# Optimization experiments

Measured on AMD Instinct MI355X. Metric: run time of the kernel, lower is better.

The kernel has to match this reference:

```python
import jax, jax.numpy as jnp
import numpy as np

N_DOMAIN = 10
DOM_EMB = 4
IN_DIM = 1024
HIDDEN = [1024, 512, 256]
N_EXPERTS = 8
LORA_R = 16


def _glorot(key, shape):
    fan_in, fan_out = shape[-2], shape[-1]
    lim = np.sqrt(6.0 / (fan_in + fan_out))
    return jax.random.uniform(key, shape, jnp.float32, -lim, lim)


def setup_inputs() -> dict:
    key = jax.random.key(0)
    ks = jax.random.split(key, 32)
    inp = {
        "dnn_input": jax.random.normal(ks[0], (16384, IN_DIM), jnp.float32),
        "domain_input": jax.random.randint(ks[1], (16384,), 0, N_DOMAIN, jnp.int64),
        "emb_table": jax.random.normal(ks[2], (N_DOMAIN, DOM_EMB), jnp.float32),
        "gate_W": _glorot(ks[3], (DOM_EMB, N_EXPERTS)),
        "gate_b": jnp.zeros((N_EXPERTS,), jnp.float32),
    }
    prev = IN_DIM
    k = 4
    for li, h in enumerate(HIDDEN):
        inp[f"W{li}"] = _glorot(ks[k], (prev, h)); k += 1
        inp[f"b{li}"] = jnp.zeros((h,), jnp.float32)
        # original inits B and lora_bias to zeros; use small randoms so outputs/grads are non-trivial
        inp[f"A{li}"] = _glorot(ks[k], (N_EXPERTS, prev, LORA_R)); k += 1
        inp[f"B{li}"] = 0.01 * jax.random.normal(ks[k], (N_EXPERTS, LORA_R, h), jnp.float32); k += 1
        inp[f"lb{li}"] = 0.01 * jax.random.normal(ks[k], (N_EXPERTS, h), jnp.float32); k += 1
        prev = h
    return inp


def _moe_layer(x, gate, W, b, A, B, lb):
    # base GEMM (dropout is identity: rate 0 / inference)
    base = x @ W + b                                   # [B, h]
    t = jnp.einsum('bp,epr->ber', x, A)                # [B, E, r]
    eo = jnp.einsum('ber,erh->beh', t, B) + lb[None]   # [B, E, h]
    moe = jnp.einsum('be,beh->bh', gate, eo)           # [B, h]
    return jax.nn.relu(base + moe)


def reference(dnn_input, domain_input, emb_table, gate_W, gate_b,
              W0, b0, A0, B0, lb0,
              W1, b1, A1, B1, lb1,
              W2, b2, A2, B2, lb2):
    dom = emb_table[domain_input]                      # [B, 4]
    gate = jax.nn.softmax(dom @ gate_W + gate_b, axis=-1)  # [B, E]
    x = dnn_input
    x = _moe_layer(x, gate, W0, b0, A0, B0, lb0)
    x = _moe_layer(x, gate, W1, b1, A1, B1, lb1)
    x = _moe_layer(x, gate, W2, b2, A2, B2, lb2)
    return x
```

## Files before the change

kernel.cpp:

```cpp
#include <hip/hip_runtime.h>
#include <hip/hip_bf16.h>
#include <stdint.h>

#define KAUG 192
#define M_ROWS 16384

typedef __attribute__((ext_vector_type(8))) __bf16 bf16x8;
typedef __attribute__((ext_vector_type(4))) float f32x4;

__device__ __forceinline__ unsigned short f2b(float f) {
  unsigned int u = __builtin_bit_cast(unsigned int, f);
  u = (u + 0x7fffu + ((u >> 16) & 1u)) >> 16;
  return (unsigned short)u;
}

__device__ __forceinline__ void lds_load16(const unsigned short* g, unsigned short* l) {
  __builtin_amdgcn_global_load_lds(
      (const __attribute__((address_space(1))) void*)g,
      (__attribute__((address_space(3))) void*)l, 16, 0, 0);
}

template<int N> __device__ __forceinline__ void vmcnt_wait() {
  if constexpr (N == 0)      asm volatile("s_waitcnt vmcnt(0)" ::: "memory");
  else if constexpr (N == 3) asm volatile("s_waitcnt vmcnt(3)" ::: "memory");
  else if constexpr (N == 4) asm volatile("s_waitcnt vmcnt(4)" ::: "memory");
  else if constexpr (N == 6) asm volatile("s_waitcnt vmcnt(6)" ::: "memory");
  else                       asm volatile("s_waitcnt vmcnt(8)" ::: "memory");
}


__global__ void gate_aug_kernel(const int* __restrict__ dom, const float* __restrict__ emb,
                                const float* __restrict__ gW, const float* __restrict__ gb,
                                float* __restrict__ gate, unsigned short* __restrict__ tg) {
  int i = blockIdx.x * blockDim.x + threadIdx.x;
  int d = dom[i];
  float e0 = emb[d*4+0], e1 = emb[d*4+1], e2 = emb[d*4+2], e3 = emb[d*4+3];
  float l[8]; float mx = -1e30f;
#pragma unroll
  for (int j = 0; j < 8; j++) {
    l[j] = e0*gW[j] + e1*gW[8+j] + e2*gW[16+j] + e3*gW[24+j] + gb[j];
    mx = fmaxf(mx, l[j]);
  }
  float s = 0.f;
#pragma unroll
  for (int j = 0; j < 8; j++) { l[j] = __expf(l[j] - mx); s += l[j]; }
  float inv = 1.0f / s;
  unsigned int g[4];
#pragma unroll
  for (int j = 0; j < 8; j++) {
    float v = l[j] * inv;
    gate[i*8+j] = v;
    unsigned int b = f2b(v);
    if (j & 1) g[j >> 1] |= b << 16; else g[j >> 1] = b;
  }
  uint4* dst = (uint4*)&tg[(long)i * KAUG + 128];
  dst[0] = make_uint4(g[0], g[1], g[2], g[3]);
  uint4 z4 = make_uint4(0, 0, 0, 0);
#pragma unroll
  for (int q = 1; q < 8; q++) dst[q] = z4;
}

__global__ void f32_to_bf16_vec(const float* __restrict__ in, unsigned int* __restrict__ out, long n8) {
  long i = (long)blockIdx.x * blockDim.x + threadIdx.x;
  if (i >= n8) return;
  float4 a = ((const float4*)in)[i * 2];
  float4 b = ((const float4*)in)[i * 2 + 1];
  uint4 o;
  o.x = f2b(a.x) | ((unsigned)f2b(a.y) << 16);
  o.y = f2b(a.z) | ((unsigned)f2b(a.w) << 16);
  o.z = f2b(b.x) | ((unsigned)f2b(b.y) << 16);
  o.w = f2b(b.z) | ((unsigned)f2b(b.w) << 16);
  ((uint4*)out)[i] = o;
}

__global__ void build_wt_all(const float* __restrict__ w0, const float* __restrict__ w1,
                             const float* __restrict__ w2,
                             unsigned short* __restrict__ t0, unsigned short* __restrict__ t1,
                             unsigned short* __restrict__ t2) {
  int z = blockIdx.z;
  const float* W = z == 0 ? w0 : (z == 1 ? w1 : w2);
  unsigned short* Wt = z == 0 ? t0 : (z == 1 ? t1 : t2);
  int K = (z == 2) ? 512 : 1024;
  int N = (z == 0) ? 1024 : (z == 1 ? 512 : 256);
  int n0 = blockIdx.x * 32, k0 = blockIdx.y * 32;
  if (n0 >= N || k0 >= K) return;
  __shared__ float tl[32][33];
  int tx = threadIdx.x & 31, ty = threadIdx.x >> 5;
#pragma unroll
  for (int i = 0; i < 32; i += 8)
    tl[ty + i][tx] = W[(long)(k0 + ty + i) * N + n0 + tx];
  __syncthreads();
#pragma unroll
  for (int i = 0; i < 32; i += 8)
    Wt[(long)(n0 + ty + i) * K + k0 + tx] = f2b(tl[tx][ty + i]);
}

__global__ void build_aft_all(const float* __restrict__ a0, const float* __restrict__ a1,
                              const float* __restrict__ a2,
                              unsigned short* __restrict__ t0, unsigned short* __restrict__ t1,
                              unsigned short* __restrict__ t2) {
  int z = blockIdx.z;
  const float* A = z == 0 ? a0 : (z == 1 ? a1 : a2);
  unsigned short* Aft = z == 0 ? t0 : (z == 1 ? t1 : t2);
  int P = (z == 2) ? 512 : 1024;
  long p0 = (long)blockIdx.x * 64;
  if (p0 >= P) return;
  int e = blockIdx.y;
  __shared__ float tl[64][17];
  int t = threadIdx.x;
#pragma unroll
  for (int pass = 0; pass < 4; pass++) {
    int idx = t + pass * 256;
    int pl = idx >> 4, r = idx & 15;
    tl[pl][r] = A[((long)e * P + p0 + pl) * 16 + r];
  }
  __syncthreads();
#pragma unroll
  for (int pass = 0; pass < 4; pass++) {
    int idx = t + pass * 256;
    int r = idx >> 6, pl = idx & 63;
    Aft[(long)(e * 16 + r) * P + p0 + pl] = f2b(tl[pl][r]);
  }
}

__global__ void build_bft_all(const float* __restrict__ b0, const float* __restrict__ b1,
                              const float* __restrict__ b2,
                              const float* __restrict__ l0, const float* __restrict__ l1,
                              const float* __restrict__ l2,
                              unsigned short* __restrict__ t0, unsigned short* __restrict__ t1,
                              unsigned short* __restrict__ t2) {
  int z = blockIdx.z;
  const float* Bm = z == 0 ? b0 : (z == 1 ? b1 : b2);
  const float* lb = z == 0 ? l0 : (z == 1 ? l1 : l2);
  unsigned short* Bft = z == 0 ? t0 : (z == 1 ? t1 : t2);
  int H = (z == 0) ? 1024 : (z == 1 ? 512 : 256);
  int n0 = blockIdx.x * 32, kk0 = blockIdx.y * 32;
  if (n0 >= H) return;
  __shared__ float tl[32][33];
  int tx = threadIdx.x & 31, ty = threadIdx.x >> 5;
#pragma unroll
  for (int i = 0; i < 32; i += 8) {
    int kk = kk0 + ty + i;
    float v;
    if (kk < 128)       v = Bm[(long)kk * H + n0 + tx];
    else if (kk < 136)  v = lb[(long)(kk - 128) * H + n0 + tx];
    else                v = 0.f;
    tl[ty + i][tx] = v;
  }
  __syncthreads();
#pragma unroll
  for (int i = 0; i < 32; i += 8)
    Bft[(long)(n0 + ty + i) * KAUG + kk0 + tx] = f2b(tl[tx][ty + i]);
}

template<int MODE, int BM>
__global__ __launch_bounds__(512)
void gemm_mn(const unsigned short* __restrict__ A1, int lda1, int K1,
             const unsigned short* __restrict__ A2, int lda2, int K2,
             const unsigned short* __restrict__ Bt1, int ldb1,
             const unsigned short* __restrict__ Bt2, int ldb2,
             const float* __restrict__ bias,
             const float* __restrict__ gate,
             void* __restrict__ outp, int ldout) {
  constexpr int MFRAG = BM / 32;
  constexpr int ATOT = BM * 64;
  constexpr int BTOT = 128 * 64;
  constexpr int LA = BM / 64;
  constexpr int L = LA + 2;
  __shared__ __attribute__((aligned(16))) unsigned short lds[3 * ATOT + 3 * BTOT];

  const int t = threadIdx.x;
  const int lane = t & 63, wave = t >> 6;
  const int wr = wave >> 2, wc = wave & 3;
  const int rl = lane & 15, kg = lane >> 4;
  const int row0 = blockIdx.x * BM, col0 = blockIdx.y * 128;

  const int sr = t >> 3;
  const int sk = ((t & 7) ^ (sr & 7)) * 8;

  f32x4 acc[MFRAG][2];
#pragma unroll
  for (int m = 0; m < MFRAG; m++)
#pragma unroll
    for (int n = 0; n < 2; n++) acc[m][n] = (f32x4){0.f, 0.f, 0.f, 0.f};

  auto stageA = [&](int buf, int kt) {
    const unsigned short* src; long ld; int kl;
    if (kt < K1) { src = A1; ld = lda1; kl = kt; }
    else         { src = A2; ld = lda2; kl = kt - K1; }
    unsigned short* d = &lds[buf * ATOT + t * 8];
    const unsigned short* s = src + (long)(row0 + sr) * ld + kl + sk;
#pragma unroll
    for (int i = 0; i < LA; i++)
      lds_load16(s + (long)(i * 64) * ld, d + i * 4096);
  };
  auto stageB = [&](int buf, int kt) {
    const unsigned short* src; long ld; int kl;
    if (kt < K1) { src = Bt1; ld = ldb1; kl = kt; }
    else         { src = Bt2; ld = ldb2; kl = kt - K1; }
    unsigned short* d = &lds[3 * ATOT + buf * BTOT + t * 8];
    const unsigned short* s = src + (long)(col0 + sr) * ld + kl + sk;
    lds_load16(s, d);
    lds_load16(s + 64 * ld, d + 4096);
  };
  auto ldA = [&](int buf, int mg, int ks) {
    int lr = wr * (BM / 2) + mg * 16 + rl;
    int sc = (ks * 4 + kg) ^ (lr & 7);
    return *(const bf16x8*)&lds[buf * ATOT + lr * 64 + sc * 8];
  };
  auto ldB = [&](int buf, int n, int ks) {
    int cr = wc * 32 + n * 16 + rl;
    int sc = (ks * 4 + kg) ^ (cr & 7);
    return *(const bf16x8*)&lds[3 * ATOT + buf * BTOT + cr * 64 + sc * 8];
  };

  const int Ktot = K1 + K2;
  const int NT = Ktot / 64;

  stageA(0, 0); stageB(0, 0);
  stageA(1, 64); stageB(1, 64);
  vmcnt_wait<L>();
  __builtin_amdgcn_s_barrier();

  int bcur = 0;
  bf16x8 Bfv[2][2];
  for (int tt = 0; tt < NT; ++tt) {
    int bpf = bcur + 2; if (bpf > 2) bpf -= 3;
    const bool pf = (tt + 2 < NT);
    bf16x8 Af[(MFRAG + 1) / 2][2];
#pragma unroll
    for (int m = 0; m < MFRAG / 2; m++) { Af[m][0] = ldA(bcur, m, 0); Af[m][1] = ldA(bcur, m, 1); }
#pragma unroll
    for (int n = 0; n < 2; n++) { Bfv[n][0] = ldB(bcur, n, 0); Bfv[n][1] = ldB(bcur, n, 1); }
    if (pf) stageA(bpf, (tt + 2) * 64);
    __builtin_amdgcn_s_barrier();
    asm volatile("s_waitcnt lgkmcnt(0)" ::: "memory");
    __builtin_amdgcn_sched_barrier(0);
    __builtin_amdgcn_s_setprio(1);
#pragma unroll
    for (int m = 0; m < MFRAG / 2; m++)
#pragma unroll
      for (int n = 0; n < 2; n++) {
        acc[m][n] = __builtin_amdgcn_mfma_f32_16x16x32_bf16(Af[m][0], Bfv[n][0], acc[m][n], 0, 0, 0);
        acc[m][n] = __builtin_amdgcn_mfma_f32_16x16x32_bf16(Af[m][1], Bfv[n][1], acc[m][n], 0, 0, 0);
      }
    __builtin_amdgcn_s_setprio(0);
    __builtin_amdgcn_s_barrier();
#pragma unroll
    for (int m = 0; m < MFRAG / 2; m++) { Af[m][0] = ldA(bcur, MFRAG / 2 + m, 0); Af[m][1] = ldA(bcur, MFRAG / 2 + m, 1); }
    if (pf) stageB(bpf, (tt + 2) * 64);
    if (tt + 1 < NT) vmcnt_wait<L>();
    else             vmcnt_wait<0>();
    __builtin_amdgcn_s_barrier();
    asm volatile("s_waitcnt lgkmcnt(0)" ::: "memory");
    __builtin_amdgcn_sched_barrier(0);
    __builtin_amdgcn_s_setprio(1);
#pragma unroll
    for (int m = 0; m < MFRAG / 2; m++)
#pragma unroll
      for (int n = 0; n < 2; n++) {
        acc[MFRAG / 2 + m][n] = __builtin_amdgcn_mfma_f32_16x16x32_bf16(Af[m][0], Bfv[n][0], acc[MFRAG / 2 + m][n], 0, 0, 0);
        acc[MFRAG / 2 + m][n] = __builtin_amdgcn_mfma_f32_16x16x32_bf16(Af[m][1], Bfv[n][1], acc[MFRAG / 2 + m][n], 0, 0, 0);
      }
    __builtin_amdgcn_s_setprio(0);
    __builtin_amdgcn_s_barrier();
    bcur = bcur == 2 ? 0 : bcur + 1;
  }

#pragma unroll
  for (int m = 0; m < MFRAG; m++)
#pragma unroll
    for (int n = 0; n < 2; n++)
#pragma unroll
      for (int j = 0; j < 4; j++) {
        int row = row0 + wr * (BM / 2) + m * 16 + kg * 4 + j;
        int col = col0 + wc * 32 + n * 16 + rl;
        float v = acc[m][n][j];
        if (MODE == 0) {
          v *= gate[row * 8 + (col >> 4)];
          ((unsigned short*)outp)[(long)row * ldout + col] = f2b(v);
        } else {
          v += bias[col];
          v = fmaxf(v, 0.f);
          if (MODE == 1) ((unsigned short*)outp)[(long)row * ldout + col] = f2b(v);
          else           ((float*)outp)[(long)row * ldout + col] = v;
        }
      }
}

template<int MODE, int BM>
__global__ __launch_bounds__(256, 4)
void gemm2b(const unsigned short* __restrict__ A1, int lda1, int K1,
            const unsigned short* __restrict__ A2, int lda2, int K2,
            const unsigned short* __restrict__ Bt1, int ldb1,
            const unsigned short* __restrict__ Bt2, int ldb2,
            const float* __restrict__ bias,
            const float* __restrict__ gate,
            void* __restrict__ outp, int ldout) {
  constexpr int ATOT = BM * 64;
  constexpr int BTOT = 128 * 64;
  constexpr int MF = BM / 64;
  constexpr int LA = BM / 32;
  __shared__ __attribute__((aligned(16))) unsigned short lds[2 * ATOT + 2 * BTOT];

  const int t = threadIdx.x;
  const int lane = t & 63, wave = t >> 6;
  const int wr = wave >> 1, wc = wave & 1;
  const int rl = lane & 15, kg = lane >> 4;
  const int row0 = blockIdx.x * BM, col0 = blockIdx.y * 128;

  const int sr = t >> 3;
  const int sk = ((t & 7) ^ (sr & 7)) * 8;

  f32x4 acc[2 * MF][4];
#pragma unroll
  for (int m = 0; m < 2 * MF; m++)
#pragma unroll
    for (int n = 0; n < 4; n++) acc[m][n] = (f32x4){0.f, 0.f, 0.f, 0.f};

  auto stageA = [&](int buf, int kt) {
    const unsigned short* src; long ld; int kl;
    if (kt < K1) { src = A1; ld = lda1; kl = kt; }
    else         { src = A2; ld = lda2; kl = kt - K1; }
    unsigned short* d = &lds[buf * ATOT + t * 8];
    const unsigned short* s = src + (long)(row0 + sr) * ld + kl + sk;
#pragma unroll
    for (int i = 0; i < LA; i++)
      lds_load16(s + (long)(i * 32) * ld, d + i * 2048);
  };
  auto stageB = [&](int buf, int kt) {
    const unsigned short* src; long ld; int kl;
    if (kt < K1) { src = Bt1; ld = ldb1; kl = kt; }
    else         { src = Bt2; ld = ldb2; kl = kt - K1; }
    unsigned short* d = &lds[2 * ATOT + buf * BTOT + t * 8];
    const unsigned short* s = src + (long)(col0 + sr) * ld + kl + sk;
#pragma unroll
    for (int i = 0; i < 4; i++)
      lds_load16(s + (long)(i * 32) * ld, d + i * 2048);
  };
  auto ldA = [&](int buf, int mf, int ks) {
    int lr = wr * (BM / 2) + mf * 16 + rl;
    int sc = (ks * 4 + kg) ^ (lr & 7);
    return *(const bf16x8*)&lds[buf * ATOT + lr * 64 + sc * 8];
  };
  auto ldB = [&](int buf, int nf, int ks) {
    int cr = wc * 64 + nf * 16 + rl;
    int sc = (ks * 4 + kg) ^ (cr & 7);
    return *(const bf16x8*)&lds[2 * ATOT + buf * BTOT + cr * 64 + sc * 8];
  };

  const int NT = (K1 + K2) / 64;

  stageA(0, 0); stageB(0, 0);
  asm volatile("s_waitcnt vmcnt(0)" ::: "memory");
  __builtin_amdgcn_s_barrier();

  int cur = 0;
  for (int tt = 0; tt < NT; ++tt) {
    const bool pf = (tt + 1 < NT);
    const int kt1 = (tt + 1) * 64;
    if (pf) { stageA(cur ^ 1, kt1); stageB(cur ^ 1, kt1); }
    bf16x8 Am_[MF][2], Bf[4][2];
#pragma unroll
    for (int mf = 0; mf < MF; mf++) { Am_[mf][0] = ldA(cur, mf, 0); Am_[mf][1] = ldA(cur, mf, 1); }
#pragma unroll
    for (int nf = 0; nf < 4; nf++) { Bf[nf][0] = ldB(cur, nf, 0); Bf[nf][1] = ldB(cur, nf, 1); }
    asm volatile("s_waitcnt lgkmcnt(0)" ::: "memory");
    __builtin_amdgcn_sched_barrier(0);
    __builtin_amdgcn_s_setprio(1);
#pragma unroll
    for (int mf = 0; mf < MF; mf++)
#pragma unroll
      for (int nf = 0; nf < 4; nf++) {
        acc[mf][nf] = __builtin_amdgcn_mfma_f32_16x16x32_bf16(Am_[mf][0], Bf[nf][0], acc[mf][nf], 0, 0, 0);
        acc[mf][nf] = __builtin_amdgcn_mfma_f32_16x16x32_bf16(Am_[mf][1], Bf[nf][1], acc[mf][nf], 0, 0, 0);
      }
    __builtin_amdgcn_s_setprio(0);
#pragma unroll
    for (int mf = 0; mf < MF; mf++) { Am_[mf][0] = ldA(cur, MF + mf, 0); Am_[mf][1] = ldA(cur, MF + mf, 1); }
    asm volatile("s_waitcnt lgkmcnt(0)" ::: "memory");
    __builtin_amdgcn_sched_barrier(0);
    __builtin_amdgcn_s_setprio(1);
#pragma unroll
    for (int mf = 0; mf < MF; mf++)
#pragma unroll
      for (int nf = 0; nf < 4; nf++) {
        acc[MF + mf][nf] = __builtin_amdgcn_mfma_f32_16x16x32_bf16(Am_[mf][0], Bf[nf][0], acc[MF + mf][nf], 0, 0, 0);
        acc[MF + mf][nf] = __builtin_amdgcn_mfma_f32_16x16x32_bf16(Am_[mf][1], Bf[nf][1], acc[MF + mf][nf], 0, 0, 0);
      }
    __builtin_amdgcn_s_setprio(0);
    if (pf) asm volatile("s_waitcnt vmcnt(0)" ::: "memory");
    __builtin_amdgcn_s_barrier();
    cur ^= 1;
  }

#pragma unroll
  for (int m = 0; m < 2 * MF; m++)
#pragma unroll
    for (int n = 0; n < 4; n++)
#pragma unroll
      for (int j = 0; j < 4; j++) {
        int row = row0 + wr * (BM / 2) + m * 16 + kg * 4 + j;
        int col = col0 + wc * 64 + n * 16 + rl;
        float v = acc[m][n][j];
        if (MODE == 0) {
          v *= gate[row * 8 + (col >> 4)];
          ((unsigned short*)outp)[(long)row * ldout + col] = f2b(v);
        } else {
          v += bias[col];
          v = fmaxf(v, 0.f);
          if (MODE == 1) ((unsigned short*)outp)[(long)row * ldout + col] = f2b(v);
          else           ((float*)outp)[(long)row * ldout + col] = v;
        }
      }
}


extern "C" void kernel_launch(void* const* d_in, const int* in_sizes, int n_in,
                              void* d_out, int out_size, void* d_ws, size_t ws_size,
                              hipStream_t stream) {
  (void)in_sizes; (void)n_in; (void)out_size; (void)ws_size;
  const float* dnn = (const float*)d_in[0];
  const int*   dom = (const int*)d_in[1];
  const float* emb = (const float*)d_in[2];
  const float* gW  = (const float*)d_in[3];
  const float* gb  = (const float*)d_in[4];
  const float* Wm[3]  = {(const float*)d_in[5],  (const float*)d_in[10], (const float*)d_in[15]};
  const float* bm[3]  = {(const float*)d_in[6],  (const float*)d_in[11], (const float*)d_in[16]};
  const float* Am[3]  = {(const float*)d_in[7],  (const float*)d_in[12], (const float*)d_in[17]};
  const float* Bm[3]  = {(const float*)d_in[8],  (const float*)d_in[13], (const float*)d_in[18]};
  const float* lbm[3] = {(const float*)d_in[9],  (const float*)d_in[14], (const float*)d_in[19]};

  const int M = M_ROWS;
  const int dIn[3]  = {1024, 1024, 512};
  const int dOutN[3] = {1024, 512, 256};

  char* p = (char*)d_ws;
  auto carve = [&](size_t bytes) { char* r = p; p += (bytes + 255) & ~(size_t)255; return r; };
  float* gate = (float*)carve((size_t)M * 8 * sizeof(float));
  unsigned short* xb0 = (unsigned short*)carve((size_t)M * 1024 * 2);
  unsigned short* xb1 = (unsigned short*)carve((size_t)M * 1024 * 2);
  unsigned short* tg  = (unsigned short*)carve((size_t)M * KAUG * 2);
  unsigned short *Wt[3], *Aft[3], *Bft[3];
  for (int l = 0; l < 3; l++) {
    Wt[l]  = (unsigned short*)carve((size_t)dOutN[l] * dIn[l] * 2);
    Aft[l] = (unsigned short*)carve((size_t)128 * dIn[l] * 2);
    Bft[l] = (unsigned short*)carve((size_t)dOutN[l] * KAUG * 2);
  }

  gate_aug_kernel<<<M / 256, 256, 0, stream>>>(dom, emb, gW, gb, gate, tg);
  {
    long n8 = (long)M * 1024 / 8;
    f32_to_bf16_vec<<<(int)((n8 + 255) / 256), 256, 0, stream>>>(dnn, (unsigned int*)xb0, n8);
  }
  build_wt_all<<<dim3(32, 32, 3), 256, 0, stream>>>(Wm[0], Wm[1], Wm[2], Wt[0], Wt[1], Wt[2]);
  build_aft_all<<<dim3(16, 8, 3), 256, 0, stream>>>(Am[0], Am[1], Am[2], Aft[0], Aft[1], Aft[2]);
  build_bft_all<<<dim3(32, KAUG / 32, 3), 256, 0, stream>>>(Bm[0], Bm[1], Bm[2],
                                                            lbm[0], lbm[1], lbm[2],
                                                            Bft[0], Bft[1], Bft[2]);

  const unsigned short* xin = xb0;
  for (int l = 0; l < 3; l++) {
    int K1 = dIn[l], N = dOutN[l];
    gemm_mn<0, 64><<<dim3(M / 64, 1), 512, 0, stream>>>(
        xin, K1, K1, nullptr, 0, 0, Aft[l], K1, nullptr, 0, nullptr, gate, (void*)tg, KAUG);
    if (l == 0)
      gemm2b<1, 128><<<dim3(M / 128, N / 128), 256, 0, stream>>>(
          xin, K1, K1, tg, KAUG, KAUG, Wt[l], K1, Bft[l], KAUG, bm[l], nullptr, (void*)xb1, N);
    else if (l == 1)
      gemm2b<1, 128><<<dim3(M / 128, N / 128), 256, 0, stream>>>(
          xin, K1, K1, tg, KAUG, KAUG, Wt[l], K1, Bft[l], KAUG, bm[l], nullptr, (void*)xb0, N);
    else
      gemm2b<2, 64><<<dim3(M / 64, N / 128), 256, 0, stream>>>(
          xin, K1, K1, tg, KAUG, KAUG, Wt[l], K1, Bft[l], KAUG, bm[l], nullptr, d_out, N);
    xin = (l == 0) ? xb1 : xb0;
  }
}
```

Before: 139.7 us.

## Fuse fp32-to-bf16 input conversion into layer-0 GEMM A-tile staging

Removes the standalone fp32-to-bf16 conversion kernel for the input and instead has both layer-0 GEMMs (LoRA-A projection and base+LoRA-B GEMM) load fp32 rows, convert them in registers, and store bf16 into LDS. This is meant to eliminate the intermediate bf16 buffer write/read and one launch. In exchange, the A-tile staging becomes synchronous register-path loads with full __syncthreads instead of async global-to-LDS loads, occupancy is lowered, and the fp32 input is read at double width by multiple column blocks.

```diff
diff --git a/kernel.cpp b/kernel.cpp
--- a/kernel.cpp
+++ b/kernel.cpp
@@ -58,19 +58,6 @@
   uint4 z4 = make_uint4(0, 0, 0, 0);
 #pragma unroll
   for (int q = 1; q < 8; q++) dst[q] = z4;
-}
-
-__global__ void f32_to_bf16_vec(const float* __restrict__ in, unsigned int* __restrict__ out, long n8) {
-  long i = (long)blockIdx.x * blockDim.x + threadIdx.x;
-  if (i >= n8) return;
-  float4 a = ((const float4*)in)[i * 2];
-  float4 b = ((const float4*)in)[i * 2 + 1];
-  uint4 o;
-  o.x = f2b(a.x) | ((unsigned)f2b(a.y) << 16);
-  o.y = f2b(a.z) | ((unsigned)f2b(a.w) << 16);
-  o.z = f2b(b.x) | ((unsigned)f2b(b.y) << 16);
-  o.w = f2b(b.z) | ((unsigned)f2b(b.w) << 16);
-  ((uint4*)out)[i] = o;
 }
 
 __global__ void build_wt_all(const float* __restrict__ w0, const float* __restrict__ w1,
@@ -288,15 +275,16 @@
       }
 }
 
-template<int MODE, int BM>
-__global__ __launch_bounds__(256, 4)
+template<int MODE, int BM, bool F32A>
+__global__ __launch_bounds__(256, F32A ? 2 : 4)
 void gemm2b(const unsigned short* __restrict__ A1, int lda1, int K1,
             const unsigned short* __restrict__ A2, int lda2, int K2,
             const unsigned short* __restrict__ Bt1, int ldb1,
             const unsigned short* __restrict__ Bt2, int ldb2,
             const float* __restrict__ bias,
             const float* __restrict__ gate,
-            void* __restrict__ outp, int ldout) {
+            void* __restrict__ outp, int ldout,
+            const float* __restrict__ Af32) {
   constexpr int ATOT = BM * 64;
   constexpr int BTOT = 128 * 64;
   constexpr int MF = BM / 64;
@@ -319,10 +307,28 @@
     for (int n = 0; n < 4; n++) acc[m][n] = (f32x4){0.f, 0.f, 0.f, 0.f};
 
   auto stageA = [&](int buf, int kt) {
+    unsigned short* d = &lds[buf * ATOT + t * 8];
+    if constexpr (F32A) {
+      if (kt < K1) {
+        const float* s = Af32 + (long)(row0 + sr) * lda1 + kt + sk;
+#pragma unroll
+        for (int i = 0; i < LA; i++) {
+          const float* sp = s + (long)(i * 32) * lda1;
+          float4 a = *(const float4*)sp;
+          float4 b = *(const float4*)(sp + 4);
+          uint4 o;
+          o.x = f2b(a.x) | ((unsigned)f2b(a.y) << 16);
+          o.y = f2b(a.z) | ((unsigned)f2b(a.w) << 16);
+          o.z = f2b(b.x) | ((unsigned)f2b(b.y) << 16);
+          o.w = f2b(b.z) | ((unsigned)f2b(b.w) << 16);
+          *(uint4*)(d + i * 2048) = o;
+        }
+        return;
+      }
+    }
     const unsigned short* src; long ld; int kl;
     if (kt < K1) { src = A1; ld = lda1; kl = kt; }
     else         { src = A2; ld = lda2; kl = kt - K1; }
-    unsigned short* d = &lds[buf * ATOT + t * 8];
     const unsigned short* s = src + (long)(row0 + sr) * ld + kl + sk;
 #pragma unroll
     for (int i = 0; i < LA; i++)
@@ -352,8 +358,7 @@
   const int NT = (K1 + K2) / 64;
 
   stageA(0, 0); stageB(0, 0);
-  asm volatile("s_waitcnt vmcnt(0)" ::: "memory");
-  __builtin_amdgcn_s_barrier();
+  __syncthreads();
 
   int cur = 0;
   for (int tt = 0; tt < NT; ++tt) {
@@ -389,8 +394,12 @@
         acc[MF + mf][nf] = __builtin_amdgcn_mfma_f32_16x16x32_bf16(Am_[mf][1], Bf[nf][1], acc[MF + mf][nf], 0, 0, 0);
       }
     __builtin_amdgcn_s_setprio(0);
-    if (pf) asm volatile("s_waitcnt vmcnt(0)" ::: "memory");
-    __builtin_amdgcn_s_barrier();
+    if constexpr (F32A) {
+      __syncthreads();
+    } else {
+      if (pf) asm volatile("s_waitcnt vmcnt(0)" ::: "memory");
+      __builtin_amdgcn_s_barrier();
+    }
     cur ^= 1;
   }
 
@@ -449,30 +458,26 @@
   }
 
   gate_aug_kernel<<<M / 256, 256, 0, stream>>>(dom, emb, gW, gb, gate, tg);
-  {
-    long n8 = (long)M * 1024 / 8;
-    f32_to_bf16_vec<<<(int)((n8 + 255) / 256), 256, 0, stream>>>(dnn, (unsigned int*)xb0, n8);
-  }
   build_wt_all<<<dim3(32, 32, 3), 256, 0, stream>>>(Wm[0], Wm[1], Wm[2], Wt[0], Wt[1], Wt[2]);
   build_aft_all<<<dim3(16, 8, 3), 256, 0, stream>>>(Am[0], Am[1], Am[2], Aft[0], Aft[1], Aft[2]);
   build_bft_all<<<dim3(32, KAUG / 32, 3), 256, 0, stream>>>(Bm[0], Bm[1], Bm[2],
                                                             lbm[0], lbm[1], lbm[2],
                                                             Bft[0], Bft[1], Bft[2]);
 
-  const unsigned short* xin = xb0;
-  for (int l = 0; l < 3; l++) {
-    int K1 = dIn[l], N = dOutN[l];
-    gemm_mn<0, 64><<<dim3(M / 64, 1), 512, 0, stream>>>(
-        xin, K1, K1, nullptr, 0, 0, Aft[l], K1, nullptr, 0, nullptr, gate, (void*)tg, KAUG);
-    if (l == 0)
-      gemm2b<1, 128><<<dim3(M / 128, N / 128), 256, 0, stream>>>(
-          xin, K1, K1, tg, KAUG, KAUG, Wt[l], K1, Bft[l], KAUG, bm[l], nullptr, (void*)xb1, N);
-    else if (l == 1)
-      gemm2b<1, 128><<<dim3(M / 128, N / 128), 256, 0, stream>>>(
-          xin, K1, K1, tg, KAUG, KAUG, Wt[l], K1, Bft[l], KAUG, bm[l], nullptr, (void*)xb0, N);
-    else
-      gemm2b<2, 64><<<dim3(M / 64, N / 128), 256, 0, stream>>>(
-          xin, K1, K1, tg, KAUG, KAUG, Wt[l], K1, Bft[l], KAUG, bm[l], nullptr, d_out, N);
-    xin = (l == 0) ? xb1 : xb0;
-  }
-}
+  gemm2b<0, 64, true><<<dim3(M / 64, 1), 256, 0, stream>>>(
+      nullptr, 1024, 1024, nullptr, 0, 0, Aft[0], 1024, nullptr, 0,
+      nullptr, gate, (void*)tg, KAUG, dnn);
+  gemm2b<1, 128, true><<<dim3(M / 128, 1024 / 128), 256, 0, stream>>>(
+      nullptr, 1024, 1024, tg, KAUG, KAUG, Wt[0], 1024, Bft[0], KAUG,
+      bm[0], nullptr, (void*)xb1, 1024, dnn);
+  gemm_mn<0, 64><<<dim3(M / 64, 1), 512, 0, stream>>>(
+      xb1, 1024, 1024, nullptr, 0, 0, Aft[1], 1024, nullptr, 0, nullptr, gate, (void*)tg, KAUG);
+  gemm2b<1, 128, false><<<dim3(M / 128, 512 / 128), 256, 0, stream>>>(
+      xb1, 1024, 1024, tg, KAUG, KAUG, Wt[1], 1024, Bft[1], KAUG,
+      bm[1], nullptr, (void*)xb0, 512, nullptr);
+  gemm_mn<0, 64><<<dim3(M / 64, 1), 512, 0, stream>>>(
+      xb0, 512, 512, nullptr, 0, 0, Aft[2], 512, nullptr, 0, nullptr, gate, (void*)tg, KAUG);
+  gemm2b<2, 64, false><<<dim3(M / 64, 256 / 128), 256, 0, stream>>>(
+      xb0, 512, 512, tg, KAUG, KAUG, Wt[2], 512, Bft[2], KAUG,
+      bm[2], nullptr, d_out, 256, nullptr);
+}
```

Result: slower. 153.3 us (+9.8%).
